# Kernel tuning notes

Hardware: AMD Instinct MI355X
Metric: run time of the kernel (lower is better)

## Reference

```python
import jax, jax.numpy as jnp
import numpy as np

N, E, IN, OUT, ED = 100000, 1600000, 64, 64, 16
NEG = -1000000000.0


def setup_inputs() -> dict:
    key = jax.random.key(0)
    ks = jax.random.split(key, 8)
    x = jax.random.normal(ks[0], (N, IN), jnp.float32)
    edge_index = jax.random.randint(ks[1], (2, E), 0, N, dtype=jnp.int32)
    edge_attr = jax.random.normal(ks[2], (E, ED), jnp.float32)
    # xavier-ish init for linear weights (stored as [in, out] for x @ W)
    Wn = jax.random.normal(ks[3], (IN, OUT), jnp.float32) * (1.0 / np.sqrt(IN))
    We = jax.random.normal(ks[4], (ED, OUT), jnp.float32) * (1.0 / np.sqrt(ED))
    att_src = jax.random.normal(ks[5], (OUT,), jnp.float32) * 0.02
    att_dst = jax.random.normal(ks[6], (OUT,), jnp.float32) * 0.02
    att_edge = jax.random.normal(ks[7], (OUT,), jnp.float32) * 0.02
    return {"x": x, "edge_index": edge_index, "edge_attr": edge_attr,
            "Wn": Wn, "We": We, "att_src": att_src, "att_dst": att_dst,
            "att_edge": att_edge}


def reference(x, edge_index, edge_attr, Wn, We, att_src, att_dst, att_edge):
    src, dst = edge_index[0], edge_index[1]
    n = x.shape[0]
    z = x @ Wn                      # [N, OUT]
    e = edge_attr @ We              # [E, OUT]
    # per-edge attention logits
    s_src = (z @ att_src)[src]      # [E]
    s_dst = (z @ att_dst)[dst]      # [E]
    s_edge = e @ att_edge           # [E]
    score = jax.nn.leaky_relu(s_src + s_dst + s_edge, negative_slope=0.2)
    # scatter softmax over dst segments (stable; matches torch amax with -1e9 init)
    max_per = jnp.maximum(jax.ops.segment_max(score, dst, num_segments=n), NEG)
    score_exp = jnp.exp(score - max_per[dst])
    denom = jax.ops.segment_sum(score_exp, dst, num_segments=n)
    alpha = score_exp / (denom[dst] + 1e-8)   # [E]
    # message + scatter-add aggregation; dropout is identity (p=0 / eval)
    msg = (z[src] + e) * alpha[:, None]       # [E, OUT]
    out = jax.ops.segment_sum(msg, dst, num_segments=n)
    # residual: in_dim == out_dim -> Identity
    return out + x
```

## Files before the change

### kernel.cpp

```cpp
#include <hip/hip_runtime.h>
#include <hip/hip_bf16.h>
#include <math.h>


__device__ __forceinline__ float bf2f(unsigned short u) {
  return __uint_as_float(((unsigned)u) << 16);
}
__device__ __forceinline__ float rdlane(float v, int k) {
  return __uint_as_float(
      (unsigned)__builtin_amdgcn_readlane((int)__float_as_uint(v), k));
}
__device__ __forceinline__ float wave_sum64(float v) {
#pragma unroll
  for (int o = 32; o > 0; o >>= 1) v += __shfl_xor(v, o);
  return v;
}

__global__ __launch_bounds__(256) void k_init(
    const float* __restrict__ Wn, const float* __restrict__ We,
    const float* __restrict__ att_src, const float* __restrict__ att_dst,
    const float* __restrict__ att_edge, float* __restrict__ vs,
    float* __restrict__ vd, float* __restrict__ weA, int* __restrict__ total,
    int* __restrict__ count, int n) {
  int i = blockIdx.x * 256 + threadIdx.x;
  for (int j = i; j < n; j += gridDim.x * 256) count[j] = 0;
  if (blockIdx.x == 0) {
    int t = threadIdx.x;
    if (t < 64) {
      float a = 0.f, b = 0.f;
#pragma unroll
      for (int c = 0; c < 64; ++c) {
        a = fmaf(Wn[t * 64 + c], att_src[c], a);
        b = fmaf(Wn[t * 64 + c], att_dst[c], b);
      }
      vs[t] = a;
      vd[t] = b;
    } else if (t < 80) {
      float a = 0.f;
#pragma unroll
      for (int c = 0; c < 64; ++c) a = fmaf(We[(t - 64) * 64 + c], att_edge[c], a);
      weA[t - 64] = a;
    } else if (t == 80) {
      *total = 0;
    }
  }
}

__global__ __launch_bounds__(256) void k_work(
    const int* __restrict__ dst, int* __restrict__ count, int* __restrict__ pos,
    int e, const float* __restrict__ x, const float* __restrict__ Wn,
    const float* __restrict__ vs, const float* __restrict__ vd,
    unsigned short* __restrict__ zb, float* __restrict__ zs,
    float* __restrict__ zd, int n, int nbe, int nbg) {
  const int b = (int)blockIdx.x;
  if (b < nbe) {
    int i = b * 256 + threadIdx.x;
    const int stride = nbe * 256;
    for (; i < e; i += stride) pos[i] = atomicAdd(&count[dst[i]], 1);
  } else if (b < nbe + nbg) {
    const int lane = threadIdx.x & 63;
    const int wid = ((b - nbe) * 256 + threadIdx.x) >> 6;
    const int nw = nbg * 4;
    float wn[64];
#pragma unroll
    for (int k = 0; k < 64; ++k) wn[k] = Wn[k * 64 + lane];
    for (int r = wid; r < n; r += nw) {
      const int ru = __builtin_amdgcn_readfirstlane(r);
      const float* xr = x + (size_t)ru * 64;
      float a0 = 0.f, a1 = 0.f, a2 = 0.f, a3 = 0.f;
#pragma unroll
      for (int k = 0; k < 64; k += 4) {
        a0 = fmaf(xr[k], wn[k], a0);
        a1 = fmaf(xr[k + 1], wn[k + 1], a1);
        a2 = fmaf(xr[k + 2], wn[k + 2], a2);
        a3 = fmaf(xr[k + 3], wn[k + 3], a3);
      }
      float acc = (a0 + a1) + (a2 + a3);
      __hip_bfloat16 bb = __float2bfloat16(acc);
      zb[(size_t)ru * 64 + lane] = *reinterpret_cast<unsigned short*>(&bb);
    }
  } else {
    int r = (b - nbe - nbg) * 256 + threadIdx.x;
    if (r >= n) return;
    const float4* xr = (const float4*)(x + (size_t)r * 64);
    const float4* vs4 = (const float4*)vs;
    const float4* vd4 = (const float4*)vd;
    float s = 0.f, d = 0.f;
#pragma unroll
    for (int j = 0; j < 16; ++j) {
      float4 q = xr[j];
      float4 a = vs4[j], bb = vd4[j];
      s = fmaf(q.x, a.x, fmaf(q.y, a.y, fmaf(q.z, a.z, fmaf(q.w, a.w, s))));
      d = fmaf(q.x, bb.x, fmaf(q.y, bb.y, fmaf(q.z, bb.z, fmaf(q.w, bb.w, d))));
    }
    zs[r] = s;
    zd[r] = d;
  }
}

__global__ __launch_bounds__(256) void k_offsets(const int* __restrict__ count,
                                                 int* __restrict__ start,
                                                 int* __restrict__ total, int n) {
  __shared__ int sdata[256];
  __shared__ int sbase;
  const int tid = threadIdx.x;
  const int i = blockIdx.x * 256 + tid;
  int c = (i < n) ? count[i] : 0;
  int v = c;
  sdata[tid] = v;
  __syncthreads();
  for (int off = 1; off < 256; off <<= 1) {
    int t = (tid >= off) ? sdata[tid - off] : 0;
    __syncthreads();
    v += t;
    sdata[tid] = v;
    __syncthreads();
  }
  if (tid == 255) sbase = atomicAdd(total, v);
  __syncthreads();
  if (i < n) start[i] = sbase + (v - c);
}

__global__ __launch_bounds__(256) void k_scatter(
    const int* __restrict__ src, const int* __restrict__ dst,
    const int* __restrict__ pos, const float* __restrict__ zs,
    const float* __restrict__ zd, const float* __restrict__ ea,
    const float* __restrict__ weA, const int* __restrict__ start,
    uint4* __restrict__ es, int e) {
  int i = blockIdx.x * 256 + threadIdx.x;
  if (i >= e) return;
  int s = src[i], d = dst[i], p = pos[i];
  size_t slot = (size_t)start[d] + p;
  const float4* eap = (const float4*)(ea + (size_t)i * 16);
  float4 q0 = eap[0], q1 = eap[1], q2 = eap[2], q3 = eap[3];
  float sed = q0.x * weA[0] + q0.y * weA[1] + q0.z * weA[2] + q0.w * weA[3] +
              q1.x * weA[4] + q1.y * weA[5] + q1.z * weA[6] + q1.w * weA[7] +
              q2.x * weA[8] + q2.y * weA[9] + q2.z * weA[10] + q2.w * weA[11] +
              q3.x * weA[12] + q3.y * weA[13] + q3.z * weA[14] + q3.w * weA[15];
  float sv = zs[s] + zd[d] + sed;
  float sc = (sv > 0.f) ? sv : 0.2f * sv;
  es[slot] = make_uint4((unsigned)s, __float_as_uint(sc), (unsigned)i, 0u);
}

__global__ __launch_bounds__(256) void k_agg(
    const float* __restrict__ x, const unsigned short* __restrict__ zb,
    const float* __restrict__ ea, const float* __restrict__ We,
    const int* __restrict__ start, const int* __restrict__ count,
    const uint4* __restrict__ es, float* __restrict__ out, int n) {
  const int lane = threadIdx.x & 63;
  const int grp = lane >> 4;
  const int gl = lane & 15;
  const int nw = (gridDim.x * blockDim.x) >> 6;
  int d = (blockIdx.x * blockDim.x + threadIdx.x) >> 6;
  if (d >= n) return;

  int s0 = start[d], cnt = count[d];
  while (d < n) {
    int dn = d + nw, sn0 = 0, cn = 0;
    if (dn < n) {
      sn0 = start[dn];
      cn = count[dn];
    }

    const int q0 = (cnt * grp) >> 2;
    const int q1 = (cnt * (grp + 1)) >> 2;

    float dsum = 0.f, ag = 0.f;
    float4 msg = make_float4(0.f, 0.f, 0.f, 0.f);

    for (int t = q0; t < q1; t += 4) {
      uint4 h[4];
      float w[4];
      ushort4 zr[4];
      float av[4];
#pragma unroll
      for (int j = 0; j < 4; ++j) {
        int tt = t + j;
        tt = (tt < q1) ? tt : (q1 - 1);
        h[j] = es[(size_t)s0 + tt];
      }
#pragma unroll
      for (int j = 0; j < 4; ++j) {
        zr[j] = *(const ushort4*)(zb + (size_t)h[j].x * 64 + gl * 4);
        av[j] = ea[(size_t)h[j].z * 16 + gl];
      }
#pragma unroll
      for (int j = 0; j < 4; ++j)
        w[j] = (t + j < q1) ? __expf(__uint_as_float(h[j].y)) : 0.f;
#pragma unroll
      for (int j = 0; j < 4; ++j) {
        dsum += w[j];
        msg.x = fmaf(w[j], bf2f(zr[j].x), msg.x);
        msg.y = fmaf(w[j], bf2f(zr[j].y), msg.y);
        msg.z = fmaf(w[j], bf2f(zr[j].z), msg.z);
        msg.w = fmaf(w[j], bf2f(zr[j].w), msg.w);
        ag = fmaf(w[j], av[j], ag);
      }
    }

    dsum += __shfl_xor(dsum, 16);
    dsum += __shfl_xor(dsum, 32);
    msg.x += __shfl_xor(msg.x, 16); msg.x += __shfl_xor(msg.x, 32);
    msg.y += __shfl_xor(msg.y, 16); msg.y += __shfl_xor(msg.y, 32);
    msg.z += __shfl_xor(msg.z, 16); msg.z += __shfl_xor(msg.z, 32);
    msg.w += __shfl_xor(msg.w, 16); msg.w += __shfl_xor(msg.w, 32);
    ag += __shfl_xor(ag, 16);
    ag += __shfl_xor(ag, 32);

    const float4* We4 = (const float4*)We;
    float4 evec = make_float4(0.f, 0.f, 0.f, 0.f);
#pragma unroll
    for (int k = 0; k < 16; ++k) {
      float agk = rdlane(ag, k);
      float4 wef = We4[k * 16 + gl];
      evec.x = fmaf(agk, wef.x, evec.x);
      evec.y = fmaf(agk, wef.y, evec.y);
      evec.z = fmaf(agk, wef.z, evec.z);
      evec.w = fmaf(agk, wef.w, evec.w);
    }

    if (grp == 0) {
      float inv = 1.f / (dsum + 1e-8f);
      const float4 xr = *(const float4*)(x + (size_t)d * 64 + gl * 4);
      float4 r;
      r.x = fmaf(msg.x + evec.x, inv, xr.x);
      r.y = fmaf(msg.y + evec.y, inv, xr.y);
      r.z = fmaf(msg.z + evec.z, inv, xr.z);
      r.w = fmaf(msg.w + evec.w, inv, xr.w);
      *(float4*)(out + (size_t)d * 64 + gl * 4) = r;
    }

    d = dn; s0 = sn0; cnt = cn;
  }
}

extern "C" void kernel_launch(void* const* d_in, const int* in_sizes, int n_in,
                              void* d_out, int out_size, void* d_ws, size_t ws_size,
                              hipStream_t stream) {
  const float* x = (const float*)d_in[0];
  const int* ei = (const int*)d_in[1];
  const float* ea = (const float*)d_in[2];
  const float* Wn = (const float*)d_in[3];
  const float* We = (const float*)d_in[4];
  const float* att_src = (const float*)d_in[5];
  const float* att_dst = (const float*)d_in[6];
  const float* att_edge = (const float*)d_in[7];
  float* out = (float*)d_out;

  const int N = in_sizes[0] / 64;
  const int E = in_sizes[1] / 2;
  const int* src = ei;
  const int* dst = ei + E;

  char* p = (char*)d_ws;
  auto carve = [&](size_t bytes) {
    void* q = (void*)p;
    p += (bytes + 255) & ~(size_t)255;
    return q;
  };
  unsigned short* zb = (unsigned short*)carve((size_t)N * 64 * 2);
  float* zs = (float*)carve((size_t)N * sizeof(float));
  float* zd = (float*)carve((size_t)N * sizeof(float));
  int* count = (int*)carve((size_t)N * sizeof(int));
  int* startp = (int*)carve((size_t)N * sizeof(int));
  int* pos = (int*)carve((size_t)E * sizeof(int));
  float* weA = (float*)carve(64);
  float* vs = (float*)carve(256);
  float* vd = (float*)carve(256);
  int* total = (int*)carve(64);
  uint4* es = (uint4*)carve((size_t)E * 16);

  const int nbe = 2048;
  const int nbg = 2048;
  const int nbz = (N + 255) / 256;
  k_init<<<256, 256, 0, stream>>>(Wn, We, att_src, att_dst, att_edge, vs, vd,
                                  weA, total, count, N);
  k_work<<<nbe + nbg + nbz, 256, 0, stream>>>(dst, count, pos, E, x, Wn, vs, vd,
                                              zb, zs, zd, N, nbe, nbg);
  k_offsets<<<(N + 255) / 256, 256, 0, stream>>>(count, startp, total, N);
  k_scatter<<<(E + 255) / 256, 256, 0, stream>>>(src, dst, pos, zs, zd, ea, weA,
                                                 startp, es, E);
  k_agg<<<4096, 256, 0, stream>>>(x, zb, ea, We, startp, count, es, out, N);
}
```

Measured before the change: 237.7 us.

## Move node GEMM into scatter kernel and prefetch next node's edges in aggregation

The bf16 z = x@Wn GEMM is moved out of the atomic counting kernel and co-scheduled with the edge scatter kernel, so it overlaps with the scatter's memory traffic instead of competing with the atomics. The aggregation kernel now launches one 64-thread block per node slot (16384 blocks) and software-prefetches the first edge records of the next destination node while processing the current one. This is meant to hide the latency of the dependent es load chain, at the cost of more registers and clamped extra loads.

```diff
diff --git a/kernel.cpp b/kernel.cpp
--- a/kernel.cpp
+++ b/kernel.cpp
@@ -9,11 +9,6 @@
 __device__ __forceinline__ float rdlane(float v, int k) {
   return __uint_as_float(
       (unsigned)__builtin_amdgcn_readlane((int)__float_as_uint(v), k));
-}
-__device__ __forceinline__ float wave_sum64(float v) {
-#pragma unroll
-  for (int o = 32; o > 0; o >>= 1) v += __shfl_xor(v, o);
-  return v;
 }
 
 __global__ __launch_bounds__(256) void k_init(
@@ -46,41 +41,18 @@
   }
 }
 
-__global__ __launch_bounds__(256) void k_work(
+__global__ __launch_bounds__(256) void k_cntzsd(
     const int* __restrict__ dst, int* __restrict__ count, int* __restrict__ pos,
-    int e, const float* __restrict__ x, const float* __restrict__ Wn,
-    const float* __restrict__ vs, const float* __restrict__ vd,
-    unsigned short* __restrict__ zb, float* __restrict__ zs,
-    float* __restrict__ zd, int n, int nbe, int nbg) {
+    int e, const float* __restrict__ x, const float* __restrict__ vs,
+    const float* __restrict__ vd, float* __restrict__ zs,
+    float* __restrict__ zd, int n, int nbe) {
   const int b = (int)blockIdx.x;
   if (b < nbe) {
     int i = b * 256 + threadIdx.x;
     const int stride = nbe * 256;
     for (; i < e; i += stride) pos[i] = atomicAdd(&count[dst[i]], 1);
-  } else if (b < nbe + nbg) {
-    const int lane = threadIdx.x & 63;
-    const int wid = ((b - nbe) * 256 + threadIdx.x) >> 6;
-    const int nw = nbg * 4;
-    float wn[64];
-#pragma unroll
-    for (int k = 0; k < 64; ++k) wn[k] = Wn[k * 64 + lane];
-    for (int r = wid; r < n; r += nw) {
-      const int ru = __builtin_amdgcn_readfirstlane(r);
-      const float* xr = x + (size_t)ru * 64;
-      float a0 = 0.f, a1 = 0.f, a2 = 0.f, a3 = 0.f;
-#pragma unroll
-      for (int k = 0; k < 64; k += 4) {
-        a0 = fmaf(xr[k], wn[k], a0);
-        a1 = fmaf(xr[k + 1], wn[k + 1], a1);
-        a2 = fmaf(xr[k + 2], wn[k + 2], a2);
-        a3 = fmaf(xr[k + 3], wn[k + 3], a3);
-      }
-      float acc = (a0 + a1) + (a2 + a3);
-      __hip_bfloat16 bb = __float2bfloat16(acc);
-      zb[(size_t)ru * 64 + lane] = *reinterpret_cast<unsigned short*>(&bb);
-    }
   } else {
-    int r = (b - nbe - nbg) * 256 + threadIdx.x;
+    int r = (b - nbe) * 256 + threadIdx.x;
     if (r >= n) return;
     const float4* xr = (const float4*)(x + (size_t)r * 64);
     const float4* vs4 = (const float4*)vs;
@@ -121,49 +93,92 @@
   if (i < n) start[i] = sbase + (v - c);
 }
 
-__global__ __launch_bounds__(256) void k_scatter(
+__global__ __launch_bounds__(256) void k_scatgemm(
     const int* __restrict__ src, const int* __restrict__ dst,
     const int* __restrict__ pos, const float* __restrict__ zs,
     const float* __restrict__ zd, const float* __restrict__ ea,
     const float* __restrict__ weA, const int* __restrict__ start,
-    uint4* __restrict__ es, int e) {
-  int i = blockIdx.x * 256 + threadIdx.x;
-  if (i >= e) return;
-  int s = src[i], d = dst[i], p = pos[i];
-  size_t slot = (size_t)start[d] + p;
-  const float4* eap = (const float4*)(ea + (size_t)i * 16);
-  float4 q0 = eap[0], q1 = eap[1], q2 = eap[2], q3 = eap[3];
-  float sed = q0.x * weA[0] + q0.y * weA[1] + q0.z * weA[2] + q0.w * weA[3] +
-              q1.x * weA[4] + q1.y * weA[5] + q1.z * weA[6] + q1.w * weA[7] +
-              q2.x * weA[8] + q2.y * weA[9] + q2.z * weA[10] + q2.w * weA[11] +
-              q3.x * weA[12] + q3.y * weA[13] + q3.z * weA[14] + q3.w * weA[15];
-  float sv = zs[s] + zd[d] + sed;
-  float sc = (sv > 0.f) ? sv : 0.2f * sv;
-  es[slot] = make_uint4((unsigned)s, __float_as_uint(sc), (unsigned)i, 0u);
-}
-
-__global__ __launch_bounds__(256) void k_agg(
+    uint4* __restrict__ es, int e, const float* __restrict__ x,
+    const float* __restrict__ Wn, unsigned short* __restrict__ zb, int n,
+    int nbs, int nbg) {
+  const int b = (int)blockIdx.x;
+  if (b < nbs) {
+    int i = b * 256 + threadIdx.x;
+    if (i >= e) return;
+    int s = src[i], d = dst[i], p = pos[i];
+    size_t slot = (size_t)start[d] + p;
+    const float4* eap = (const float4*)(ea + (size_t)i * 16);
+    float4 q0 = eap[0], q1 = eap[1], q2 = eap[2], q3 = eap[3];
+    float sed = q0.x * weA[0] + q0.y * weA[1] + q0.z * weA[2] + q0.w * weA[3] +
+                q1.x * weA[4] + q1.y * weA[5] + q1.z * weA[6] + q1.w * weA[7] +
+                q2.x * weA[8] + q2.y * weA[9] + q2.z * weA[10] + q2.w * weA[11] +
+                q3.x * weA[12] + q3.y * weA[13] + q3.z * weA[14] + q3.w * weA[15];
+    float sv = zs[s] + zd[d] + sed;
+    float sc = (sv > 0.f) ? sv : 0.2f * sv;
+    es[slot] = make_uint4((unsigned)s, __float_as_uint(sc), (unsigned)i, 0u);
+  } else {
+    const int lane = threadIdx.x & 63;
+    const int wid = ((b - nbs) * 256 + threadIdx.x) >> 6;
+    const int nw = nbg * 4;
+    float wn[64];
+#pragma unroll
+    for (int k = 0; k < 64; ++k) wn[k] = Wn[k * 64 + lane];
+    for (int r = wid; r < n; r += nw) {
+      const int ru = __builtin_amdgcn_readfirstlane(r);
+      const float* xr = x + (size_t)ru * 64;
+      float a0 = 0.f, a1 = 0.f, a2 = 0.f, a3 = 0.f;
+#pragma unroll
+      for (int k = 0; k < 64; k += 4) {
+        a0 = fmaf(xr[k], wn[k], a0);
+        a1 = fmaf(xr[k + 1], wn[k + 1], a1);
+        a2 = fmaf(xr[k + 2], wn[k + 2], a2);
+        a3 = fmaf(xr[k + 3], wn[k + 3], a3);
+      }
+      float acc = (a0 + a1) + (a2 + a3);
+      __hip_bfloat16 bb = __float2bfloat16(acc);
+      zb[(size_t)ru * 64 + lane] = *reinterpret_cast<unsigned short*>(&bb);
+    }
+  }
+}
+
+__global__ __launch_bounds__(64) void k_agg(
     const float* __restrict__ x, const unsigned short* __restrict__ zb,
     const float* __restrict__ ea, const float* __restrict__ We,
     const int* __restrict__ start, const int* __restrict__ count,
-    const uint4* __restrict__ es, float* __restrict__ out, int n) {
+    const uint4* __restrict__ es, float* __restrict__ out, int n, int e) {
   const int lane = threadIdx.x & 63;
   const int grp = lane >> 4;
   const int gl = lane & 15;
-  const int nw = (gridDim.x * blockDim.x) >> 6;
-  int d = (blockIdx.x * blockDim.x + threadIdx.x) >> 6;
+  const int nw = gridDim.x;
+  int d = blockIdx.x;
   if (d >= n) return;
+  const int emax = e - 1;
 
   int s0 = start[d], cnt = count[d];
-  while (d < n) {
-    int dn = d + nw, sn0 = 0, cn = 0;
-    if (dn < n) {
+  int q0 = (cnt * grp) >> 2;
+  int q1 = (cnt * (grp + 1)) >> 2;
+  uint4 hp[4];
+#pragma unroll
+  for (int j = 0; j < 4; ++j) {
+    int tt = min(q0 + j, q1 - 1); tt = max(tt, 0);
+    hp[j] = es[min((size_t)(s0 + tt), (size_t)emax)];
+  }
+
+  while (true) {
+    int dn = d + nw, sn0 = 0, cn = 0, qn0 = 0, qn1 = 0;
+    uint4 hpn[4];
+    const bool more = dn < n;
+    if (more) {
       sn0 = start[dn];
       cn = count[dn];
-    }
-
-    const int q0 = (cnt * grp) >> 2;
-    const int q1 = (cnt * (grp + 1)) >> 2;
+      qn0 = (cn * grp) >> 2;
+      qn1 = (cn * (grp + 1)) >> 2;
+#pragma unroll
+      for (int j = 0; j < 4; ++j) {
+        int tt = min(qn0 + j, qn1 - 1); tt = max(tt, 0);
+        hpn[j] = es[min((size_t)(sn0 + tt), (size_t)emax)];
+      }
+    }
 
     float dsum = 0.f, ag = 0.f;
     float4 msg = make_float4(0.f, 0.f, 0.f, 0.f);
@@ -173,11 +188,12 @@
       float w[4];
       ushort4 zr[4];
       float av[4];
-#pragma unroll
-      for (int j = 0; j < 4; ++j) {
-        int tt = t + j;
-        tt = (tt < q1) ? tt : (q1 - 1);
-        h[j] = es[(size_t)s0 + tt];
+      if (t == q0) {
+#pragma unroll
+        for (int j = 0; j < 4; ++j) h[j] = hp[j];
+      } else {
+#pragma unroll
+        for (int j = 0; j < 4; ++j) h[j] = es[(size_t)s0 + min(t + j, q1 - 1)];
       }
 #pragma unroll
       for (int j = 0; j < 4; ++j) {
@@ -230,7 +246,10 @@
       *(float4*)(out + (size_t)d * 64 + gl * 4) = r;
     }
 
-    d = dn; s0 = sn0; cnt = cn;
+    if (!more) break;
+    d = dn; s0 = sn0; cnt = cn; q0 = qn0; q1 = qn1;
+#pragma unroll
+    for (int j = 0; j < 4; ++j) hp[j] = hpn[j];
   }
 }
 
@@ -271,14 +290,16 @@
   uint4* es = (uint4*)carve((size_t)E * 16);
 
   const int nbe = 2048;
+  const int nbz = (N + 255) / 256;
+  const int nbs = (E + 255) / 256;
   const int nbg = 2048;
-  const int nbz = (N + 255) / 256;
   k_init<<<256, 256, 0, stream>>>(Wn, We, att_src, att_dst, att_edge, vs, vd,
                                   weA, total, count, N);
-  k_work<<<nbe + nbg + nbz, 256, 0, stream>>>(dst, count, pos, E, x, Wn, vs, vd,
-                                              zb, zs, zd, N, nbe, nbg);
+  k_cntzsd<<<nbe + nbz, 256, 0, stream>>>(dst, count, pos, E, x, vs, vd, zs, zd,
+                                          N, nbe);
   k_offsets<<<(N + 255) / 256, 256, 0, stream>>>(count, startp, total, N);
-  k_scatter<<<(E + 255) / 256, 256, 0, stream>>>(src, dst, pos, zs, zd, ea, weA,
-                                                 startp, es, E);
-  k_agg<<<4096, 256, 0, stream>>>(x, zb, ea, We, startp, count, es, out, N);
-}
+  k_scatgemm<<<nbs + nbg, 256, 0, stream>>>(src, dst, pos, zs, zd, ea, weA,
+                                            startp, es, E, x, Wn, zb, N, nbs,
+                                            nbg);
+  k_agg<<<16384, 64, 0, stream>>>(x, zb, ea, We, startp, count, es, out, N, E);
+}
```

Measured after the change: 244.3 us. +2.8%, slower.
